# Kernel tuning notes

Measured on AMD Instinct MI355X. Metric: run time of the kernel, lower is better.

Reference implementation:

```python
import jax, jax.numpy as jnp
import numpy as np

QMIN, QMAX = -128.0, 127.0
LEVELS = 255.0


def setup_inputs() -> dict:
    key = jax.random.key(0)
    k1, k2, k3 = jax.random.split(key, 3)
    N, IN, OUT = 16384, 4096, 4096
    x = jax.random.normal(k1, (N, IN), dtype=jnp.float32)
    weight = jax.random.normal(k2, (OUT, IN), dtype=jnp.float32) * 0.02
    bias = jax.random.normal(k3, (OUT,), dtype=jnp.float32) * 0.02
    return {"x": x, "weight": weight, "bias": bias}


def _quant_act(x):
    # asymmetric, per-tensor int8 quantization (min-max)
    mn = jnp.minimum(jnp.min(x), 0.0)
    mx = jnp.maximum(jnp.max(x), 0.0)
    sc = (mx - mn) / LEVELS
    zp = jnp.round(QMIN - mn / sc)
    q = jnp.clip(jnp.round(x / sc) + zp, QMIN, QMAX)
    return q, sc, zp


def reference(x, weight, bias):
    # --- weight quant: symmetric, per-channel (channel_dim=0) ---
    w_scale = jnp.max(jnp.abs(weight), axis=1) / QMAX  # [O]
    qw = jnp.clip(jnp.round(weight / w_scale[:, None]), -QMAX, QMAX)  # [O, I]

    # --- activation quant: asymmetric, per-tensor ---
    qx, sc, zp = _quant_act(x)
    qx = qx - zp  # zero-point subtraction (QLayer.forward)

    # --- integer GEMM (simulated in fp32): res32 = (qx - zp) @ qw.T ---
    res32 = jnp.einsum('ni,oi->no', qx, qw)

    # --- bias requantized into int32 accumulator domain ---
    qbias = jnp.round(bias[None, :] / (w_scale[None, :] * sc))  # [1, O]
    res32 = res32 + qbias

    # --- requantization params from res32 (per-tensor, per_channel=False) ---
    rmn = jnp.minimum(jnp.min(res32), 0.0)
    rmx = jnp.maximum(jnp.max(res32), 0.0)
    re_sc = (rmx - rmn) / LEVELS
    re_zp = jnp.round(QMIN - rmn / re_sc)
    res8 = jnp.clip(jnp.round(res32 / re_sc) + re_zp, QMIN, QMAX)

    # --- combined dequant scale: sc * w_scale * re_sc, then dequantize ---
    out_scale = sc * w_scale[None, :] * re_sc  # [1, O]
    return (res8 - re_zp) * out_scale
```

## Files before the change

### kernel.cpp

```cpp
#include <hip/hip_runtime.h>
#include <climits>
#include <cstdint>

#define N_ROWS 16384
#define K_DIM  4096
#define O_DIM  4096

typedef __attribute__((ext_vector_type(4))) int int4v;
typedef __attribute__((address_space(1))) void gvoid;
typedef __attribute__((address_space(3))) void svoid;


__device__ __forceinline__ unsigned enc_f(float f) {
  unsigned u = __float_as_uint(f);
  return (u & 0x80000000u) ? ~u : (u | 0x80000000u);
}
__device__ __forceinline__ float dec_f(unsigned u) {
  unsigned b = (u & 0x80000000u) ? (u & 0x7FFFFFFFu) : ~u;
  return __uint_as_float(b);
}

__device__ __forceinline__ void gload16(const void* g, void* l) {
  __builtin_amdgcn_global_load_lds((gvoid*)g, (svoid*)l, 16, 0, 0);
}

__global__ void k_init(unsigned* s) {
  s[0] = 0xFFFFFFFFu;
  s[1] = 0u;
  ((int*)s)[2] = INT_MAX;
  ((int*)s)[3] = INT_MIN;
}

__global__ void k_minmax_x(const float4* __restrict__ x, unsigned* s, int n4) {
  const int tid = threadIdx.x;
  float lmn = 3.402823466e38f, lmx = -3.402823466e38f;
  for (int i = blockIdx.x * blockDim.x + tid; i < n4; i += gridDim.x * blockDim.x) {
    float4 v = x[i];
    lmn = fminf(lmn, fminf(fminf(v.x, v.y), fminf(v.z, v.w)));
    lmx = fmaxf(lmx, fmaxf(fmaxf(v.x, v.y), fmaxf(v.z, v.w)));
  }
  __shared__ float smn[256], smx[256];
  smn[tid] = lmn; smx[tid] = lmx;
  __syncthreads();
  for (int st = 128; st > 0; st >>= 1) {
    if (tid < st) {
      smn[tid] = fminf(smn[tid], smn[tid + st]);
      smx[tid] = fmaxf(smx[tid], smx[tid + st]);
    }
    __syncthreads();
  }
  if (tid == 0) {
    atomicMin(&s[0], enc_f(smn[0]));
    atomicMax(&s[1], enc_f(smx[0]));
  }
}

__global__ void k_scalar_a(unsigned* s) {
  float mn = fminf(dec_f(s[0]), 0.0f);
  float mx = fmaxf(dec_f(s[1]), 0.0f);
  float sc = (mx - mn) / 255.0f;
  float zp = rintf(-128.0f - mn / sc);
  float* f = (float*)s;
  f[4] = sc;
  f[5] = zp;
}

__global__ void k_wquant(const float* __restrict__ w, char* __restrict__ qw,
                         float* __restrict__ w_scale, int* __restrict__ colsum) {
  const int o = blockIdx.x, tid = threadIdx.x;
  const float4* row = (const float4*)(w + (size_t)o * K_DIM);
  float4 v[4];
  float ma = 0.0f;
#pragma unroll
  for (int i = 0; i < 4; i++) {
    v[i] = row[tid + i * 256];
    ma = fmaxf(ma, fmaxf(fmaxf(fabsf(v[i].x), fabsf(v[i].y)),
                         fmaxf(fabsf(v[i].z), fabsf(v[i].w))));
  }
  __shared__ float red[256];
  red[tid] = ma;
  __syncthreads();
  for (int st = 128; st > 0; st >>= 1) {
    if (tid < st) red[tid] = fmaxf(red[tid], red[tid + st]);
    __syncthreads();
  }
  __shared__ float wsb;
  if (tid == 0) {
    wsb = red[0] / 127.0f;
    w_scale[o] = wsb;
  }
  __syncthreads();
  const float wsc = wsb;
  uint32_t* qrow = (uint32_t*)(qw + (size_t)o * K_DIM);
  int lsum = 0;
#pragma unroll
  for (int i = 0; i < 4; i++) {
    const float* pv = (const float*)&v[i];
    uint32_t pk = 0;
#pragma unroll
    for (int c = 0; c < 4; c++) {
      float qf = rintf(pv[c] / wsc);
      qf = fminf(fmaxf(qf, -127.0f), 127.0f);
      int qi = (int)qf;
      lsum += qi;
      pk |= (uint32_t)(unsigned char)(signed char)qi << (8 * c);
    }
    qrow[tid + i * 256] = pk;
  }
  __shared__ int ired[256];
  ired[tid] = lsum;
  __syncthreads();
  for (int st = 128; st > 0; st >>= 1) {
    if (tid < st) ired[tid] += ired[tid + st];
    __syncthreads();
  }
  if (tid == 0) colsum[o] = ired[0];
}

__global__ void k_corr(const float* __restrict__ bias, const float* __restrict__ w_scale,
                       int* corr, const float* __restrict__ s) {
  const int o = blockIdx.x * blockDim.x + threadIdx.x;
  if (o >= O_DIM) return;
  const float sc = s[4];
  const int zp = (int)s[5];
  const int cs = corr[o];
  const float qb = rintf(bias[o] / (w_scale[o] * sc));
  corr[o] = (int)qb - zp * cs;
}

__global__ void k_xquant(const float4* __restrict__ x, uint32_t* __restrict__ qx,
                         const float* __restrict__ s, int n4) {
  const float sc = s[4], zp = s[5];
  for (int i = blockIdx.x * blockDim.x + threadIdx.x; i < n4;
       i += gridDim.x * blockDim.x) {
    float4 v = x[i];
    const float* pv = (const float*)&v;
    uint32_t pk = 0;
#pragma unroll
    for (int c = 0; c < 4; c++) {
      float qf = rintf(pv[c] / sc) + zp;
      qf = fminf(fmaxf(qf, -128.0f), 127.0f);
      pk |= (uint32_t)(unsigned char)(signed char)(int)qf << (8 * c);
    }
    qx[i] = pk;
  }
}

__global__ __launch_bounds__(256) void k_gemm(
    const char* __restrict__ qx, const char* __restrict__ qw,
    int* __restrict__ C, const int* __restrict__ corr, int* rm) {
  __shared__ int4v As[128 * 4];
  __shared__ int4v Bs[128 * 4];

  const int tid = threadIdx.x;
  const int lane = tid & 63;
  const int wave = tid >> 6;
  const int q = lane >> 4;
  const int r_ = lane & 15;
  const int wm = (wave >> 1) * 64;
  const int wn = (wave & 1) * 64;
  const long bm = (long)blockIdx.y * 128;
  const long bo = (long)blockIdx.x * 128;

  const int srow = tid >> 2;
  const int scol = (tid & 3) * 16;
  const char* gA = qx + (bm + srow) * (long)K_DIM + scol;
  const char* gB = qw + (bo + srow) * (long)K_DIM + scol;
  char* lA = (char*)As + tid * 16;
  char* lB = (char*)Bs + tid * 16;

  int4v acc[4][4];
#pragma unroll
  for (int a = 0; a < 4; a++)
#pragma unroll
    for (int b = 0; b < 4; b++) acc[a][b] = (int4v){0, 0, 0, 0};

  for (int k0 = 0; k0 < K_DIM; k0 += 64) {
    gload16(gA + k0, lA);
    gload16(gA + (long)64 * K_DIM + k0, lA + 4096);
    gload16(gB + k0, lB);
    gload16(gB + (long)64 * K_DIM + k0, lB + 4096);
    __syncthreads();

    int4v af[4], bf[4];
#pragma unroll
    for (int mt = 0; mt < 4; mt++) af[mt] = As[(wm + mt * 16 + r_) * 4 + q];
#pragma unroll
    for (int nt = 0; nt < 4; nt++) bf[nt] = Bs[(wn + nt * 16 + r_) * 4 + q];
#pragma unroll
    for (int mt = 0; mt < 4; mt++)
#pragma unroll
      for (int nt = 0; nt < 4; nt++)
        acc[mt][nt] = __builtin_amdgcn_mfma_i32_16x16x64_i8(
            af[mt], bf[nt], acc[mt][nt], 0, 0, 0);
    __syncthreads();
  }

  int lmin = INT_MAX, lmax = INT_MIN;
#pragma unroll
  for (int nt = 0; nt < 4; nt++) {
    const int col = (int)bo + wn + nt * 16 + r_;
    const int cr = corr[col];
#pragma unroll
    for (int mt = 0; mt < 4; mt++) {
#pragma unroll
      for (int rr = 0; rr < 4; rr++) {
        const long row = bm + wm + mt * 16 + q * 4 + rr;
        const int v = acc[mt][nt][rr] + cr;
        C[row * O_DIM + col] = v;
        lmin = min(lmin, v);
        lmax = max(lmax, v);
      }
    }
  }
  int* red = (int*)As;
  red[tid] = lmin;
  red[256 + tid] = lmax;
  __syncthreads();
  for (int st = 128; st > 0; st >>= 1) {
    if (tid < st) {
      red[tid] = min(red[tid], red[tid + st]);
      red[256 + tid] = max(red[256 + tid], red[256 + tid + st]);
    }
    __syncthreads();
  }
  if (tid == 0) {
    atomicMin(&rm[2], red[0]);
    atomicMax(&rm[3], red[256]);
  }
}

__global__ void k_scalar_b(unsigned* s) {
  float rmn = fminf((float)((int*)s)[2], 0.0f);
  float rmx = fmaxf((float)((int*)s)[3], 0.0f);
  float re_sc = (rmx - rmn) / 255.0f;
  float re_zp = rintf(-128.0f - rmn / re_sc);
  float* f = (float*)s;
  f[6] = re_sc;
  f[7] = re_zp;
}

__global__ void k_requant(int4* ci, float4* co, const float* __restrict__ w_scale,
                          const float* __restrict__ s, int n4) {
  const float sc = s[4], re_sc = s[6], re_zp = s[7];
  const float4* wsv4 = (const float4*)w_scale;
  for (int i = blockIdx.x * blockDim.x + threadIdx.x; i < n4;
       i += gridDim.x * blockDim.x) {
    int4 r = ci[i];
    float4 wv = wsv4[i & (O_DIM / 4 - 1)];
    float4 o;
    {
      float v = rintf((float)r.x / re_sc) + re_zp;
      v = fminf(fmaxf(v, -128.0f), 127.0f);
      o.x = (v - re_zp) * ((sc * wv.x) * re_sc);
    }
    {
      float v = rintf((float)r.y / re_sc) + re_zp;
      v = fminf(fmaxf(v, -128.0f), 127.0f);
      o.y = (v - re_zp) * ((sc * wv.y) * re_sc);
    }
    {
      float v = rintf((float)r.z / re_sc) + re_zp;
      v = fminf(fmaxf(v, -128.0f), 127.0f);
      o.z = (v - re_zp) * ((sc * wv.z) * re_sc);
    }
    {
      float v = rintf((float)r.w / re_sc) + re_zp;
      v = fminf(fmaxf(v, -128.0f), 127.0f);
      o.w = (v - re_zp) * ((sc * wv.w) * re_sc);
    }
    co[i] = o;
  }
}

extern "C" void kernel_launch(void* const* d_in, const int* in_sizes, int n_in,
                              void* d_out, int out_size, void* d_ws, size_t ws_size,
                              hipStream_t stream) {
  const float* x = (const float*)d_in[0];
  const float* w = (const float*)d_in[1];
  const float* bias = (const float*)d_in[2];

  char* ws = (char*)d_ws;
  unsigned* s = (unsigned*)ws;
  float* w_scale = (float*)(ws + 256);
  int* corr = (int*)(ws + 32768);
  char* qw = ws + 65536;
  char* qx = ws + 65536 + (size_t)O_DIM * K_DIM;

  const int n4x = (N_ROWS * K_DIM) / 4;

  k_init<<<1, 1, 0, stream>>>(s);
  k_minmax_x<<<2048, 256, 0, stream>>>((const float4*)x, s, n4x);
  k_scalar_a<<<1, 1, 0, stream>>>(s);
  k_wquant<<<O_DIM, 256, 0, stream>>>(w, qw, w_scale, corr);
  k_corr<<<O_DIM / 256, 256, 0, stream>>>(bias, w_scale, corr, (const float*)s);
  k_xquant<<<2048, 256, 0, stream>>>((const float4*)x, (uint32_t*)qx,
                                     (const float*)s, n4x);
  dim3 g(O_DIM / 128, N_ROWS / 128);
  k_gemm<<<g, 256, 0, stream>>>(qx, qw, (int*)d_out, corr, (int*)s);
  k_scalar_b<<<1, 1, 0, stream>>>(s);
  k_requant<<<4096, 256, 0, stream>>>((int4*)d_out, (float4*)d_out, w_scale,
                                      (const float*)s, (N_ROWS * O_DIM) / 4);
}
```

Baseline: 1.067 ms.

## Restructure int8 GEMM into 256x256 tiles with triple-buffered async LDS pipeline

Rewrites the int8 MFMA GEMM to use 256x256 block tiles with 512 threads, triple-buffered LDS filled by direct global-to-LDS loads, XOR-swizzled LDS addressing and a grouped workgroup remap for L2 locality. Loads for tile t+2 are issued while MFMAs on tile t run, with split barriers and s_setprio around the compute phases. The aim is to hide global-load latency behind compute and raise arithmetic intensity per block. The costs are higher register and LDS pressure and fragile manual waitcnt accounting.

Measured after the change: 974.4 us. 1.1x faster.

```diff
diff --git a/kernel.cpp b/kernel.cpp
--- a/kernel.cpp
+++ b/kernel.cpp
@@ -23,6 +23,15 @@
 __device__ __forceinline__ void gload16(const void* g, void* l) {
   __builtin_amdgcn_global_load_lds((gvoid*)g, (svoid*)l, 16, 0, 0);
 }
+
+#define BAR()                                  \
+  do {                                         \
+    asm volatile("" ::: "memory");             \
+    __builtin_amdgcn_s_barrier();              \
+    asm volatile("" ::: "memory");             \
+  } while (0)
+
+#define MFMA_I8(a, b, c) __builtin_amdgcn_mfma_i32_16x16x64_i8(a, b, c, 0, 0, 0)
 
 __global__ void k_init(unsigned* s) {
   s[0] = 0xFFFFFFFFu;
@@ -146,87 +155,159 @@
   }
 }
 
-__global__ __launch_bounds__(256) void k_gemm(
+#define BM 256
+#define BN 256
+#define BKB 64
+#define NTILE (K_DIM / BKB)
+#define BUFB (BM * BKB)
+
+__global__ __launch_bounds__(512, 2) void k_gemm(
     const char* __restrict__ qx, const char* __restrict__ qw,
     int* __restrict__ C, const int* __restrict__ corr, int* rm) {
-  __shared__ int4v As[128 * 4];
-  __shared__ int4v Bs[128 * 4];
+  __shared__ int4v As[3 * BUFB / 16];
+  __shared__ int4v Bs[3 * BUFB / 16];
 
   const int tid = threadIdx.x;
   const int lane = tid & 63;
   const int wave = tid >> 6;
   const int q = lane >> 4;
   const int r_ = lane & 15;
-  const int wm = (wave >> 1) * 64;
-  const int wn = (wave & 1) * 64;
-  const long bm = (long)blockIdx.y * 128;
-  const long bo = (long)blockIdx.x * 128;
+  const int wm = (wave >> 2) * 128;
+  const int wn = (wave & 3) * 64;
+
+  int wg = blockIdx.y * gridDim.x + blockIdx.x;
+  wg = (wg & 7) * 128 + (wg >> 3);
+  const long bm = (long)(wg >> 4) * BM;
+  const long bo = (long)(wg & 15) * BN;
 
   const int srow = tid >> 2;
-  const int scol = (tid & 3) * 16;
-  const char* gA = qx + (bm + srow) * (long)K_DIM + scol;
-  const char* gB = qw + (bo + srow) * (long)K_DIM + scol;
+  const int scol = (((tid & 3) ^ ((tid >> 3) & 3)) << 4);
+  const char* gA0 = qx + (bm + srow) * (long)K_DIM + scol;
+  const char* gA1 = gA0 + (long)128 * K_DIM;
+  const char* gB0 = qw + (bo + srow) * (long)K_DIM + scol;
+  const char* gB1 = gB0 + (long)128 * K_DIM;
   char* lA = (char*)As + tid * 16;
   char* lB = (char*)Bs + tid * 16;
 
-  int4v acc[4][4];
-#pragma unroll
-  for (int a = 0; a < 4; a++)
-#pragma unroll
-    for (int b = 0; b < 4; b++) acc[a][b] = (int4v){0, 0, 0, 0};
-
-  for (int k0 = 0; k0 < K_DIM; k0 += 64) {
-    gload16(gA + k0, lA);
-    gload16(gA + (long)64 * K_DIM + k0, lA + 4096);
-    gload16(gB + k0, lB);
-    gload16(gB + (long)64 * K_DIM + k0, lB + 4096);
-    __syncthreads();
+  int offA[8], offB[4];
+#pragma unroll
+  for (int m = 0; m < 8; ++m) {
+    const int row = wm + m * 16 + r_;
+    const int a = row * 64 + q * 16;
+    offA[m] = a ^ (((row >> 1) & 3) << 4);
+  }
+#pragma unroll
+  for (int n = 0; n < 4; ++n) {
+    const int row = wn + n * 16 + r_;
+    const int a = row * 64 + q * 16;
+    offB[n] = a ^ (((row >> 1) & 3) << 4);
+  }
+
+  int4v acc[8][4];
+#pragma unroll
+  for (int m = 0; m < 8; ++m)
+#pragma unroll
+    for (int n = 0; n < 4; ++n) acc[m][n] = (int4v){0, 0, 0, 0};
+
+  gload16(gA0, lA);
+  gload16(gA1, lA + 8192);
+  gload16(gB0, lB);
+  gload16(gB1, lB + 8192);
+  gload16(gA0 + 64, lA + BUFB);
+  gload16(gA1 + 64, lA + BUFB + 8192);
+  gload16(gB0 + 64, lB + BUFB);
+  gload16(gB1 + 64, lB + BUFB + 8192);
+  asm volatile("s_waitcnt vmcnt(4)" ::: "memory");
+  __builtin_amdgcn_s_barrier();
+  asm volatile("" ::: "memory");
+
+  int cur = 0;
+  int gk = 128;
+  for (int t = 0; t < NTILE; ++t) {
+    const char* bA = (const char*)As + cur * BUFB;
+    const char* bB = (const char*)Bs + cur * BUFB;
+    int nxt = cur + 2;
+    if (nxt >= 3) nxt -= 3;
 
     int4v af[4], bf[4];
 #pragma unroll
-    for (int mt = 0; mt < 4; mt++) af[mt] = As[(wm + mt * 16 + r_) * 4 + q];
-#pragma unroll
-    for (int nt = 0; nt < 4; nt++) bf[nt] = Bs[(wn + nt * 16 + r_) * 4 + q];
-#pragma unroll
-    for (int mt = 0; mt < 4; mt++)
-#pragma unroll
-      for (int nt = 0; nt < 4; nt++)
-        acc[mt][nt] = __builtin_amdgcn_mfma_i32_16x16x64_i8(
-            af[mt], bf[nt], acc[mt][nt], 0, 0, 0);
-    __syncthreads();
+    for (int m = 0; m < 4; ++m) af[m] = *(const int4v*)(bA + offA[m]);
+#pragma unroll
+    for (int n = 0; n < 4; ++n) bf[n] = *(const int4v*)(bB + offB[n]);
+    if (t < NTILE - 2) {
+      char* dA = (char*)As + nxt * BUFB + tid * 16;
+      gload16(gA0 + gk, dA);
+      gload16(gA1 + gk, dA + 8192);
+    }
+    BAR();
+    __builtin_amdgcn_s_setprio(1);
+#pragma unroll
+    for (int m = 0; m < 4; ++m)
+#pragma unroll
+      for (int n = 0; n < 4; ++n)
+        acc[m][n] = MFMA_I8(af[m], bf[n], acc[m][n]);
+    __builtin_amdgcn_s_setprio(0);
+    BAR();
+
+#pragma unroll
+    for (int m = 0; m < 4; ++m) af[m] = *(const int4v*)(bA + offA[4 + m]);
+    if (t < NTILE - 2) {
+      char* dB = (char*)Bs + nxt * BUFB + tid * 16;
+      gload16(gB0 + gk, dB);
+      gload16(gB1 + gk, dB + 8192);
+    }
+    BAR();
+    __builtin_amdgcn_s_setprio(1);
+#pragma unroll
+    for (int m = 0; m < 4; ++m)
+#pragma unroll
+      for (int n = 0; n < 4; ++n)
+        acc[4 + m][n] = MFMA_I8(af[m], bf[n], acc[4 + m][n]);
+    __builtin_amdgcn_s_setprio(0);
+    if (t < NTILE - 2) {
+      asm volatile("s_waitcnt vmcnt(4)" ::: "memory");
+    } else if (t == NTILE - 2) {
+      asm volatile("s_waitcnt vmcnt(0)" ::: "memory");
+    }
+    __builtin_amdgcn_s_barrier();
+    asm volatile("" ::: "memory");
+
+    cur = cur == 2 ? 0 : cur + 1;
+    gk += 64;
   }
 
   int lmin = INT_MAX, lmax = INT_MIN;
 #pragma unroll
-  for (int nt = 0; nt < 4; nt++) {
-    const int col = (int)bo + wn + nt * 16 + r_;
+  for (int n = 0; n < 4; ++n) {
+    const int col = (int)bo + wn + n * 16 + r_;
     const int cr = corr[col];
 #pragma unroll
-    for (int mt = 0; mt < 4; mt++) {
-#pragma unroll
-      for (int rr = 0; rr < 4; rr++) {
-        const long row = bm + wm + mt * 16 + q * 4 + rr;
-        const int v = acc[mt][nt][rr] + cr;
+    for (int m = 0; m < 8; ++m) {
+#pragma unroll
+      for (int rr = 0; rr < 4; ++rr) {
+        const long row = bm + wm + m * 16 + q * 4 + rr;
+        const int v = acc[m][n][rr] + cr;
         C[row * O_DIM + col] = v;
         lmin = min(lmin, v);
         lmax = max(lmax, v);
       }
     }
   }
+  __syncthreads();
   int* red = (int*)As;
   red[tid] = lmin;
-  red[256 + tid] = lmax;
-  __syncthreads();
-  for (int st = 128; st > 0; st >>= 1) {
+  red[512 + tid] = lmax;
+  __syncthreads();
+  for (int st = 256; st > 0; st >>= 1) {
     if (tid < st) {
       red[tid] = min(red[tid], red[tid + st]);
-      red[256 + tid] = max(red[256 + tid], red[256 + tid + st]);
+      red[512 + tid] = max(red[512 + tid], red[512 + tid + st]);
     }
     __syncthreads();
   }
   if (tid == 0) {
     atomicMin(&rm[2], red[0]);
-    atomicMax(&rm[3], red[256]);
+    atomicMax(&rm[3], red[512]);
   }
 }
 
@@ -296,8 +377,8 @@
   k_corr<<<O_DIM / 256, 256, 0, stream>>>(bias, w_scale, corr, (const float*)s);
   k_xquant<<<2048, 256, 0, stream>>>((const float4*)x, (uint32_t*)qx,
                                      (const float*)s, n4x);
-  dim3 g(O_DIM / 128, N_ROWS / 128);
-  k_gemm<<<g, 256, 0, stream>>>(qx, qw, (int*)d_out, corr, (int*)s);
+  dim3 g(O_DIM / BN, N_ROWS / BM);
+  k_gemm<<<g, 512, 0, stream>>>(qx, qw, (int*)d_out, corr, (int*)s);
   k_scalar_b<<<1, 1, 0, stream>>>(s);
   k_requant<<<4096, 256, 0, stream>>>((int4*)d_out, (float4*)d_out, w_scale,
                                       (const float*)s, (N_ROWS * O_DIM) / 4);
```
